# Optimization experiments

Measured on AMD Instinct MI355X. Metric: run time of the kernel, lower is better.

## Reference

```python
import jax, jax.numpy as jnp
import numpy as np

B, DIN, E, FACTOR, STEPS, NH = 2048, 1024, 1024, 16, 3, 8
DH = E // NH
EPS = 1e-5


def layernorm(x, g, b):
    m = x.mean(-1, keepdims=True)
    v = ((x - m) ** 2).mean(-1, keepdims=True)
    return (x - m) / jnp.sqrt(v + EPS) * g + b


def setup_inputs() -> dict:
    key = jax.random.key(0)
    ks = iter(jax.random.split(key, 32))
    r = lambda shape, s=0.02: jax.random.normal(next(ks), shape, dtype=jnp.float32) * s
    F = E * FACTOR
    return {
        "image_feat": jax.random.normal(next(ks), (B, DIN), dtype=jnp.float32),
        "text_feat": jax.random.normal(next(ks), (B, DIN), dtype=jnp.float32),
        # fusion block
        "fc1_w": r((F, DIN)), "fc1_b": jnp.zeros((F,), jnp.float32),
        "fc2_w": r((F, DIN)), "fc2_b": jnp.zeros((F,), jnp.float32),
        "fc3_w": r((E, F)), "fc3_b": jnp.zeros((E,), jnp.float32),
        "ln_g": jnp.ones((E,), jnp.float32), "ln_b": jnp.zeros((E,), jnp.float32),
        # per-step MHA + FFN + norms, stacked over STEPS
        "Wqkv": r((STEPS, 3 * E, E)), "bqkv": jnp.zeros((STEPS, 3 * E), jnp.float32),
        "Wo": r((STEPS, E, E)), "bo": jnp.zeros((STEPS, E), jnp.float32),
        "W1": r((STEPS, E, E)), "b1": jnp.zeros((STEPS, E), jnp.float32),
        "W2": r((STEPS, E, E)), "b2": jnp.zeros((STEPS, E), jnp.float32),
        "n1_g": jnp.ones((STEPS, E), jnp.float32), "n1_b": jnp.zeros((STEPS, E), jnp.float32),
        "n2_g": jnp.ones((STEPS, E), jnp.float32), "n2_b": jnp.zeros((STEPS, E), jnp.float32),
        # output projection
        "Wout": r((DIN, E)), "bout": jnp.zeros((DIN,), jnp.float32),
    }


def mha_step(q, ctx, Wqkv, bqkv, Wo, bo):
    # q: [B,E] (query len 1), ctx: [B,L,E]
    Wq, Wk, Wv = Wqkv[:E], Wqkv[E:2 * E], Wqkv[2 * E:]
    bq, bk, bv = bqkv[:E], bqkv[E:2 * E], bqkv[2 * E:]
    L = ctx.shape[1]
    qh = (q @ Wq.T + bq).reshape(B, NH, DH)
    kh = (ctx @ Wk.T + bk).reshape(B, L, NH, DH)
    vh = (ctx @ Wv.T + bv).reshape(B, L, NH, DH)
    scores = jnp.einsum("bhd,blhd->bhl", qh, kh) / jnp.sqrt(jnp.float32(DH))
    attn = jax.nn.softmax(scores, axis=-1)
    out = jnp.einsum("bhl,blhd->bhd", attn, vh).reshape(B, E)
    return out @ Wo.T + bo


def reference(image_feat, text_feat, fc1_w, fc1_b, fc2_w, fc2_b, fc3_w, fc3_b,
              ln_g, ln_b, Wqkv, bqkv, Wo, bo, W1, b1, W2, b2,
              n1_g, n1_b, n2_g, n2_b, Wout, bout):
    # fusion block (dropout = identity in eval)
    fused = (image_feat @ fc1_w.T + fc1_b) * (text_feat @ fc2_w.T + fc2_b)
    fused = layernorm(fused @ fc3_w.T + fc3_b, ln_g, ln_b)  # [B,E]
    ctx = fused[:, None, :]  # [B,1,E]
    x = fused
    for i in range(STEPS):
        attn = mha_step(x, ctx, Wqkv[i], bqkv[i], Wo[i], bo[i])
        x = x + layernorm(attn, n1_g[i], n1_b[i])
        ffn = jax.nn.relu(x @ W1[i].T + b1[i]) @ W2[i].T + b2[i]
        x = x + layernorm(ffn, n2_g[i], n2_b[i])
        ctx = jnp.concatenate([ctx, x[:, None, :]], axis=1)
    final_output = x @ Wout.T + bout  # [B,DIN]
    return final_output, ctx
```

## Files before the change

### kernel.cpp

```cpp
#include <hip/hip_runtime.h>

#define TB 256

typedef __attribute__((ext_vector_type(8))) short short8;
typedef __attribute__((ext_vector_type(4))) float f32x4;
typedef unsigned short u16;

constexpr int B_  = 2048;
constexpr int DIN = 1024;
constexpr int E   = 1024;
constexpr int F   = 16384;
constexpr int E3  = 3072;
constexpr int CH  = 4096;

struct Ptr8 { void* p[8]; };

__device__ __forceinline__ u16 f2bf(float f) {
  union { float f; unsigned u; } v; v.f = f;
  unsigned r = v.u + 0x7fffu + ((v.u >> 16) & 1u);
  return (u16)(r >> 16);
}
__device__ __forceinline__ float bf2f(u16 u) {
  union { unsigned u; float f; } v; v.u = ((unsigned)u) << 16;
  return v.f;
}

__device__ __forceinline__ void gload16(const void* g, void* l) {
  __builtin_amdgcn_global_load_lds(
      (const __attribute__((address_space(1))) void*)g,
      (__attribute__((address_space(3))) void*)l, 16, 0, 0);
}

__device__ __forceinline__ void tile_xy(int& tx, int& ty) {
  int gx = gridDim.x;
  int nwg = gx * gridDim.y;
  int wg = blockIdx.y * gx + blockIdx.x;
  if ((nwg & 7) == 0) wg = (wg & 7) * (nwg >> 3) + (wg >> 3);
  tx = wg % gx; ty = wg / gx;
}

__device__ __forceinline__ int swz16(int o) {
  return o ^ (((o >> 7) & 7) << 4);
}

__global__ __launch_bounds__(256) void cvt_kernel(const float* __restrict__ s,
                                                  u16* __restrict__ d, int n) {
  int i = (blockIdx.x * 256 + threadIdx.x) * 4;
  if (i >= n) return;
  float4 v = *(const float4*)&s[i];
  ushort4 o;
  o.x = f2bf(v.x); o.y = f2bf(v.y); o.z = f2bf(v.z); o.w = f2bf(v.w);
  *(ushort4*)&d[i] = o;
}

__global__ __launch_bounds__(256) void fill_kernel(float* p, int n, float v) {
  int i = blockIdx.x * 256 + threadIdx.x;
  if (i < n) p[i] = v;
}

__global__ __launch_bounds__(256) void relu_multi_kernel(
    Ptr8 ys, int ny, const float* __restrict__ bias, u16* __restrict__ out) {
  size_t i = ((size_t)blockIdx.x * 256 + threadIdx.x) * 4;
  int col = (int)(i & 1023);
  float4 b = *(const float4*)&bias[col];
  float a0 = b.x, a1 = b.y, a2 = b.z, a3 = b.w;
  for (int j = 0; j < ny; ++j) {
    float4 z = *(const float4*)&((const float*)ys.p[j])[i];
    a0 += z.x; a1 += z.y; a2 += z.z; a3 += z.w;
  }
  ushort4 o;
  o.x = f2bf(a0 > 0.f ? a0 : 0.f);
  o.y = f2bf(a1 > 0.f ? a1 : 0.f);
  o.z = f2bf(a2 > 0.f ? a2 : 0.f);
  o.w = f2bf(a3 > 0.f ? a3 : 0.f);
  *(ushort4*)&out[i] = o;
}

__global__ __launch_bounds__(256) void combine_out_kernel(
    Ptr8 ys, int ny, const float* __restrict__ bias, float* __restrict__ out) {
  size_t i = ((size_t)blockIdx.x * 256 + threadIdx.x) * 4;
  int col = (int)(i & 1023);
  float4 b = *(const float4*)&bias[col];
  float a0 = b.x, a1 = b.y, a2 = b.z, a3 = b.w;
  for (int j = 0; j < ny; ++j) {
    float4 z = *(const float4*)&((const float*)ys.p[j])[i];
    a0 += z.x; a1 += z.y; a2 += z.z; a3 += z.w;
  }
  out[i] = a0; out[i + 1] = a1; out[i + 2] = a2; out[i + 3] = a3;
}

template <int EPI>
__global__ __launch_bounds__(512, 2) void gemm256(
    const u16* __restrict__ A, int sA,
    const u16* __restrict__ Bw, int sB,
    const float* __restrict__ bias, const u16* __restrict__ gate,
    void* __restrict__ Out, Ptr8 pouts, int ldOut, int ksz) {
  __shared__ __align__(16) char smem[131072];
  const int tid = threadIdx.x, lane = tid & 63, w = tid >> 6;
  const int wm = w >> 2, wn = w & 3;
  int tx, ty; tile_xy(tx, ty);
  const int m0 = tx * 256, n0 = ty * 256;
  const int k0 = blockIdx.z * ksz;
  const int nt = ksz >> 5;
  const int lr = lane & 15;

  f32x4 acc[8][4] = {};

  auto stage = [&](const u16* __restrict__ G, int gs, int gr0, int kk, int tb, int j) {
    int P = j * 8192 + w * 1024 + lane * 16;
    int L = swz16(P);
    int pr = L >> 7, sub = (L >> 6) & 1, kb = L & 63;
    gload16(G + (size_t)(gr0 + pr * 2 + sub) * gs + kk + (kb >> 1),
            &smem[tb + P]);
  };
  auto rdA = [&](int tb, int mf) -> short8 {
    int r = wm * 128 + mf * 16 + lr;
    int o = (r >> 1) * 128 + (r & 1) * 64 + (lane >> 4) * 16;
    return *(const short8*)&smem[tb + swz16(o)];
  };
  auto rdB = [&](int tb, int nf) -> short8 {
    int r = wn * 64 + nf * 16 + lr;
    int o = (r >> 1) * 128 + (r & 1) * 64 + (lane >> 4) * 16;
    return *(const short8*)&smem[tb + swz16(o)];
  };
  auto slotA = [](int t) { return (t & 3) * 16384; };
  auto slotB = [](int t) { return 65536 + (t & 3) * 16384; };

#pragma unroll
  for (int j = 0; j < 2; ++j) stage(A, sA, m0, k0, slotA(0), j);
#pragma unroll
  for (int j = 0; j < 2; ++j) stage(Bw, sB, n0, k0, slotB(0), j);
  if (nt > 1) {
#pragma unroll
    for (int j = 0; j < 2; ++j) stage(A, sA, m0, k0 + 32, slotA(1), j);
#pragma unroll
    for (int j = 0; j < 2; ++j) stage(Bw, sB, n0, k0 + 32, slotB(1), j);
    asm volatile("s_waitcnt vmcnt(4)" ::: "memory");
  } else {
    asm volatile("s_waitcnt vmcnt(0)" ::: "memory");
  }
  __builtin_amdgcn_sched_barrier(0);
  __builtin_amdgcn_s_barrier();

  for (int t = 0; t < nt; ++t) {
    const int sa = slotA(t), sb = slotB(t);
    if (t + 2 < nt) {
#pragma unroll
      for (int j = 0; j < 2; ++j) stage(A, sA, m0, k0 + (t + 2) * 32, slotA(t + 2), j);
#pragma unroll
      for (int j = 0; j < 2; ++j) stage(Bw, sB, n0, k0 + (t + 2) * 32, slotB(t + 2), j);
    }
    short8 afr[8], bfr[4];
#pragma unroll
    for (int nf = 0; nf < 4; ++nf) bfr[nf] = rdB(sb, nf);
#pragma unroll
    for (int mf = 0; mf < 8; ++mf) afr[mf] = rdA(sa, mf);
    __builtin_amdgcn_s_setprio(1);
#pragma unroll
    for (int mf = 0; mf < 8; ++mf)
#pragma unroll
      for (int nf = 0; nf < 4; ++nf)
        acc[mf][nf] = __builtin_amdgcn_mfma_f32_16x16x32_bf16(
            afr[mf], bfr[nf], acc[mf][nf], 0, 0, 0);
    __builtin_amdgcn_s_setprio(0);
    if (t + 2 < nt) {
      asm volatile("s_waitcnt vmcnt(4)" ::: "memory");
    } else if (t + 1 < nt) {
      asm volatile("s_waitcnt vmcnt(0)" ::: "memory");
    }
    if (t + 1 < nt) {
      __builtin_amdgcn_sched_barrier(0);
      __builtin_amdgcn_s_barrier();
    }
  }

  if (EPI == 0) {
    float* Pf = (float*)pouts.p[blockIdx.z];
    const int rb = (lane >> 4) * 4;
#pragma unroll
    for (int mf = 0; mf < 8; ++mf) {
#pragma unroll
      for (int nf = 0; nf < 4; ++nf) {
        int row0 = m0 + wm * 128 + mf * 16 + rb;
        int col  = n0 + wn * 64 + nf * 16 + lr;
#pragma unroll
        for (int r = 0; r < 4; ++r)
          Pf[(size_t)(row0 + r) * ldOut + col] = acc[mf][nf][r];
      }
    }
  } else {
    __syncthreads();
    char* wbase = smem + w * 16384;
    const int rb = (lane >> 4) * 4;
    const int g4 = lane >> 4;
#pragma unroll
    for (int mf = 0; mf < 8; ++mf) {
      char* wmf = wbase + mf * 2048;
#pragma unroll
      for (int nf = 0; nf < 4; ++nf) {
        float bv = (bias == nullptr) ? 0.f : bias[n0 + wn * 64 + nf * 16 + lr];
        int pb = nf ^ g4;
#pragma unroll
        for (int r = 0; r < 4; ++r)
          *(u16*)&wmf[(rb + r) * 128 + pb * 32 + lr * 2] =
              f2bf(acc[mf][nf][r] + bv);
      }
      asm volatile("s_waitcnt lgkmcnt(0)" ::: "memory");
      __builtin_amdgcn_sched_barrier(0);
      int rrow = lane >> 2, wb = lane & 3;
      int pb2 = wb ^ (rrow >> 2);
      short8 v0 = *(const short8*)&wmf[rrow * 128 + pb2 * 32];
      short8 v1 = *(const short8*)&wmf[rrow * 128 + pb2 * 32 + 16];
      size_t gidx = (size_t)(m0 + wm * 128 + mf * 16 + rrow) * ldOut +
                    (n0 + wn * 64 + wb * 16);
      if (EPI == 4) {
        short8 g0 = *(const short8*)&gate[gidx];
        short8 g1 = *(const short8*)&gate[gidx + 8];
        short8 o0, o1;
#pragma unroll
        for (int j = 0; j < 8; ++j) {
          o0[j] = (short)f2bf(bf2f((u16)v0[j]) * bf2f((u16)g0[j]));
          o1[j] = (short)f2bf(bf2f((u16)v1[j]) * bf2f((u16)g1[j]));
        }
        *(short8*)((u16*)Out + gidx) = o0;
        *(short8*)((u16*)Out + gidx + 8) = o1;
      } else {
        *(short8*)((u16*)Out + gidx) = v0;
        *(short8*)((u16*)Out + gidx + 8) = v1;
      }
    }
  }
}

template <int EPI>
__global__ __launch_bounds__(TB) void gemm_bt(
    const u16* __restrict__ A, int sA,
    const u16* __restrict__ Bw, int sB,
    const float* __restrict__ bias, Ptr8 outs,
    int ldOut, int Kext, int ksz) {
  __shared__ u16 As[128 * 32];
  __shared__ u16 Bs[128 * 32];
  const int tid = threadIdx.x, lane = tid & 63, w = tid >> 6;
  const int wr = w >> 1, wc = w & 1;
  int tx, ty; tile_xy(tx, ty);
  const int m0 = tx * 128, n0 = ty * 128;
  const int k0 = blockIdx.z * ksz;
  const int kend = min(k0 + ksz, Kext);

  f32x4 acc[4][4] = {};
  const int lr = lane & 15, lk = (lane >> 4) * 8;

  for (int kk = k0; kk < kend; kk += 32) {
#pragma unroll
    for (int is = 0; is < 2; ++is) {
      int c = is * 256 + tid;
      int r = c >> 2, kc = (c & 3) << 3;
      size_t lb = (size_t)(is * 256 + w * 64) * 8;
      gload16(A  + (size_t)(m0 + r) * sA + kk + kc, &As[lb]);
      gload16(Bw + (size_t)(n0 + r) * sB + kk + kc, &Bs[lb]);
    }
    __syncthreads();
    short8 af[4], bfv[4];
#pragma unroll
    for (int m = 0; m < 4; ++m)
      af[m] = *(const short8*)&As[(wr * 64 + m * 16 + lr) * 32 + lk];
#pragma unroll
    for (int n = 0; n < 4; ++n)
      bfv[n] = *(const short8*)&Bs[(wc * 64 + n * 16 + lr) * 32 + lk];
#pragma unroll
    for (int m = 0; m < 4; ++m)
#pragma unroll
      for (int n = 0; n < 4; ++n)
        acc[m][n] = __builtin_amdgcn_mfma_f32_16x16x32_bf16(af[m], bfv[n], acc[m][n], 0, 0, 0);
    __syncthreads();
  }

  float* Of = (float*)outs.p[EPI == 0 ? blockIdx.z : 0];
  const int rbase = (lane >> 4) * 4;
#pragma unroll
  for (int m = 0; m < 4; ++m) {
#pragma unroll
    for (int n = 0; n < 4; ++n) {
      int row0 = m0 + wr * 64 + m * 16 + rbase;
      int col  = n0 + wc * 64 + n * 16 + lr;
      float bv = (bias == nullptr) ? 0.f : bias[col];
#pragma unroll
      for (int r = 0; r < 4; ++r) {
        float v = acc[m][n][r] + bv;
        size_t idx = (size_t)(row0 + r) * ldOut + col;
        if (EPI == 0) Of[idx] = v;
        else          ((u16*)Of)[idx] = f2bf(v);
      }
    }
  }
}

template <int EPI>
__global__ __launch_bounds__(TB) void gemm_wf32(
    const u16* __restrict__ A, int sA,
    const float* __restrict__ Bw, int sB,
    const float* __restrict__ bias, void* __restrict__ Out, int ldOut,
    int Kext, int ksz) {
  __shared__ u16 As[128 * 32];
  __shared__ u16 Bs[128 * 32];
  const int tid = threadIdx.x, lane = tid & 63, w = tid >> 6;
  const int wr = w >> 1, wc = w & 1;
  int tx, ty; tile_xy(tx, ty);
  const int m0 = tx * 128, n0 = ty * 128;
  const int k0 = blockIdx.z * ksz;
  const int kend = min(k0 + ksz, Kext);

  f32x4 acc[4][4] = {};
  const int lr = lane & 15, lk = (lane >> 4) * 8;

  for (int kk = k0; kk < kend; kk += 32) {
#pragma unroll
    for (int is = 0; is < 2; ++is) {
      int c = is * 256 + tid;
      int r = c >> 2, kc = (c & 3) << 3;
      gload16(A + (size_t)(m0 + r) * sA + kk + kc,
              &As[(size_t)(is * 256 + w * 64) * 8]);
    }
#pragma unroll
    for (int p = 0; p < 4; ++p) {
      int t = tid + p * 256;
      int r = t >> 3, c4 = (t & 7) << 2;
      float4 v = *(const float4*)&Bw[(size_t)(n0 + r) * sB + kk + c4];
      ushort4 o;
      o.x = f2bf(v.x); o.y = f2bf(v.y); o.z = f2bf(v.z); o.w = f2bf(v.w);
      *(ushort4*)&Bs[r * 32 + c4] = o;
    }
    __syncthreads();
    short8 af[4], bfv[4];
#pragma unroll
    for (int m = 0; m < 4; ++m)
      af[m] = *(const short8*)&As[(wr * 64 + m * 16 + lr) * 32 + lk];
#pragma unroll
    for (int n = 0; n < 4; ++n)
      bfv[n] = *(const short8*)&Bs[(wc * 64 + n * 16 + lr) * 32 + lk];
#pragma unroll
    for (int m = 0; m < 4; ++m)
#pragma unroll
      for (int n = 0; n < 4; ++n)
        acc[m][n] = __builtin_amdgcn_mfma_f32_16x16x32_bf16(af[m], bfv[n], acc[m][n], 0, 0, 0);
    __syncthreads();
  }

  const int rbase = (lane >> 4) * 4;
#pragma unroll
  for (int m = 0; m < 4; ++m) {
#pragma unroll
    for (int n = 0; n < 4; ++n) {
      int row0 = m0 + wr * 64 + m * 16 + rbase;
      int col  = n0 + wc * 64 + n * 16 + lr;
      float bv = (EPI == 3 || bias == nullptr) ? 0.f : bias[col];
#pragma unroll
      for (int r = 0; r < 4; ++r) {
        float v = acc[m][n][r] + bv;
        size_t idx = (size_t)(row0 + r) * ldOut + col;
        if (EPI == 0)      ((float*)Out)[idx] = v;
        else if (EPI == 1) ((u16*)Out)[idx] = f2bf(v);
        else if (EPI == 2) ((u16*)Out)[idx] = f2bf(v > 0.f ? v : 0.f);
        else               atomicAdd((float*)Out + idx, v);
      }
    }
  }
}

__global__ __launch_bounds__(TB) void gemm_dual_wf32(
    const u16* __restrict__ A1, const u16* __restrict__ A2, int sA,
    const float* __restrict__ B1, const float* __restrict__ B2, int sB,
    const float* __restrict__ bias1, const float* __restrict__ bias2,
    u16* __restrict__ Out, int ldOut, int K) {
  __shared__ u16 As1[128 * 32];
  __shared__ u16 As2[128 * 32];
  __shared__ u16 Bs1[128 * 32];
  __shared__ u16 Bs2[128 * 32];
  const int tid = threadIdx.x, lane = tid & 63, w = tid >> 6;
  const int wr = w >> 1, wc = w & 1;
  int tx, ty; tile_xy(tx, ty);
  const int m0 = tx * 128, n0 = ty * 128;

  f32x4 acc1[4][4] = {};
  f32x4 acc2[4][4] = {};
  const int lr = lane & 15, lk = (lane >> 4) * 8;

  for (int kk = 0; kk < K; kk += 32) {
#pragma unroll
    for (int is = 0; is < 2; ++is) {
      int c = is * 256 + tid;
      int r = c >> 2, kc = (c & 3) << 3;
      size_t lb = (size_t)(is * 256 + w * 64) * 8;
      gload16(A1 + (size_t)(m0 + r) * sA + kk + kc, &As1[lb]);
      gload16(A2 + (size_t)(m0 + r) * sA + kk + kc, &As2[lb]);
    }
#pragma unroll
    for (int p = 0; p < 4; ++p) {
      int t = tid + p * 256;
      int r = t >> 3, c4 = (t & 7) << 2;
      float4 v1 = *(const float4*)&B1[(size_t)(n0 + r) * sB + kk + c4];
      float4 v2 = *(const float4*)&B2[(size_t)(n0 + r) * sB + kk + c4];
      ushort4 o1, o2;
      o1.x = f2bf(v1.x); o1.y = f2bf(v1.y); o1.z = f2bf(v1.z); o1.w = f2bf(v1.w);
      o2.x = f2bf(v2.x); o2.y = f2bf(v2.y); o2.z = f2bf(v2.z); o2.w = f2bf(v2.w);
      *(ushort4*)&Bs1[r * 32 + c4] = o1;
      *(ushort4*)&Bs2[r * 32 + c4] = o2;
    }
    __syncthreads();
    short8 a1[4], a2[4], b1v[4], b2v[4];
#pragma unroll
    for (int m = 0; m < 4; ++m) {
      a1[m] = *(const short8*)&As1[(wr * 64 + m * 16 + lr) * 32 + lk];
      a2[m] = *(const short8*)&As2[(wr * 64 + m * 16 + lr) * 32 + lk];
    }
#pragma unroll
    for (int n = 0; n < 4; ++n) {
      b1v[n] = *(const short8*)&Bs1[(wc * 64 + n * 16 + lr) * 32 + lk];
      b2v[n] = *(const short8*)&Bs2[(wc * 64 + n * 16 + lr) * 32 + lk];
    }
#pragma unroll
    for (int m = 0; m < 4; ++m)
#pragma unroll
      for (int n = 0; n < 4; ++n) {
        acc1[m][n] = __builtin_amdgcn_mfma_f32_16x16x32_bf16(a1[m], b1v[n], acc1[m][n], 0, 0, 0);
        acc2[m][n] = __builtin_amdgcn_mfma_f32_16x16x32_bf16(a2[m], b2v[n], acc2[m][n], 0, 0, 0);
      }
    __syncthreads();
  }

  const int rbase = (lane >> 4) * 4;
#pragma unroll
  for (int m = 0; m < 4; ++m) {
#pragma unroll
    for (int n = 0; n < 4; ++n) {
      int row0 = m0 + wr * 64 + m * 16 + rbase;
      int col  = n0 + wc * 64 + n * 16 + lr;
      float bv1 = bias1[col], bv2 = bias2[col];
#pragma unroll
      for (int r = 0; r < 4; ++r) {
        float v = (acc1[m][n][r] + bv1) * (acc2[m][n][r] + bv2);
        Out[(size_t)(row0 + r) * ldOut + col] = f2bf(v);
      }
    }
  }
}

template <int MODE>
__global__ __launch_bounds__(256) void resln_kernel(
    Ptr8 ys, int ny, const float* __restrict__ preb,
    const float* __restrict__ g, const float* __restrict__ bp,
    float* __restrict__ x, u16* __restrict__ xb,
    float* __restrict__ ctxo, int ctxRow) {
  const int r = blockIdx.x, tid = threadIdx.x;
  const size_t base = (size_t)r * 1024 + tid * 4;
  float y[4] = {0.f, 0.f, 0.f, 0.f};
  for (int j = 0; j < ny; ++j) {
    float4 z = *(const float4*)&((const float*)ys.p[j])[base];
    y[0] += z.x; y[1] += z.y; y[2] += z.z; y[3] += z.w;
  }
  if (preb != nullptr) {
    float4 p4 = *(const float4*)&preb[tid * 4];
    y[0] += p4.x; y[1] += p4.y; y[2] += p4.z; y[3] += p4.w;
  }
  float s = y[0] + y[1] + y[2] + y[3];
  float q = y[0] * y[0] + y[1] * y[1] + y[2] * y[2] + y[3] * y[3];
  __shared__ float red[8];
  for (int o = 32; o; o >>= 1) { s += __shfl_xor(s, o); q += __shfl_xor(q, o); }
  int wv = tid >> 6;
  if ((tid & 63) == 0) { red[wv] = s; red[4 + wv] = q; }
  __syncthreads();
  s = red[0] + red[1] + red[2] + red[3];
  q = red[4] + red[5] + red[6] + red[7];
  float mean = s * (1.f / 1024.f);
  float var  = q * (1.f / 1024.f) - mean * mean;
  float rs   = rsqrtf(var + 1e-5f);
  float4 g4 = *(const float4*)&g[tid * 4];
  float4 b4 = *(const float4*)&bp[tid * 4];
  float gg[4] = {g4.x, g4.y, g4.z, g4.w};
  float bb[4] = {b4.x, b4.y, b4.z, b4.w};
  float xv[4];
#pragma unroll
  for (int j = 0; j < 4; ++j) {
    float val = (y[j] - mean) * rs * gg[j] + bb[j];
    xv[j] = (MODE == 0) ? val : x[base + j] + val;
  }
  *(float4*)&x[base] = make_float4(xv[0], xv[1], xv[2], xv[3]);
  ushort4 xo;
  xo.x = f2bf(xv[0]); xo.y = f2bf(xv[1]); xo.z = f2bf(xv[2]); xo.w = f2bf(xv[3]);
  *(ushort4*)&xb[base] = xo;
  if (MODE != 1) {
    size_t cb = ((size_t)r * 4 + ctxRow) * 1024 + tid * 4;
    *(float4*)&ctxo[cb] = make_float4(xv[0], xv[1], xv[2], xv[3]);
  }
}

__global__ __launch_bounds__(64) void attn_kernel(
    const u16* __restrict__ q, int qstride,
    const u16* __restrict__ kv, int kvstride, int voff,
    u16* __restrict__ out, int L) {
  const int b = blockIdx.x >> 3, h = blockIdx.x & 7;
  const int lane = threadIdx.x;
  const size_t qoff = (size_t)b * qstride + h * 128;
  float q0 = bf2f(q[qoff + lane]);
  float q1 = bf2f(q[qoff + 64 + lane]);
  float sc[3];
  for (int l = 0; l < L; ++l) {
    size_t kb = ((size_t)l * B_ + b) * kvstride + h * 128;
    float p = q0 * bf2f(kv[kb + lane]) + q1 * bf2f(kv[kb + 64 + lane]);
    for (int o = 32; o; o >>= 1) p += __shfl_xor(p, o);
    sc[l] = p * 0.08838834764831843f;
  }
  float m = sc[0];
  for (int l = 1; l < L; ++l) m = fmaxf(m, sc[l]);
  float wsum = 0.f, wgt[3];
  for (int l = 0; l < L; ++l) { wgt[l] = expf(sc[l] - m); wsum += wgt[l]; }
  float inv = 1.f / wsum;
  float o0 = 0.f, o1 = 0.f;
  for (int l = 0; l < L; ++l) {
    size_t vb = ((size_t)l * B_ + b) * kvstride + voff + h * 128;
    o0 += wgt[l] * bf2f(kv[vb + lane]);
    o1 += wgt[l] * bf2f(kv[vb + 64 + lane]);
  }
  out[(size_t)b * 1024 + h * 128 + lane]      = f2bf(o0 * inv);
  out[(size_t)b * 1024 + h * 128 + 64 + lane] = f2bf(o1 * inv);
}

extern "C" void kernel_launch(void* const* d_in, const int* in_sizes, int n_in,
                              void* d_out, int out_size, void* d_ws, size_t ws_size,
                              hipStream_t stream) {
  (void)in_sizes; (void)n_in;
  const float* image = (const float*)d_in[0];
  const float* text  = (const float*)d_in[1];
  const float* fc1_w = (const float*)d_in[2];
  const float* fc1_b = (const float*)d_in[3];
  const float* fc2_w = (const float*)d_in[4];
  const float* fc2_b = (const float*)d_in[5];
  const float* fc3_w = (const float*)d_in[6];
  const float* fc3_b = (const float*)d_in[7];
  const float* ln_g  = (const float*)d_in[8];
  const float* ln_b  = (const float*)d_in[9];
  const float* Wqkv  = (const float*)d_in[10];
  const float* bqkv  = (const float*)d_in[11];
  const float* Wo    = (const float*)d_in[12];
  const float* bo    = (const float*)d_in[13];
  const float* W1    = (const float*)d_in[14];
  const float* b1    = (const float*)d_in[15];
  const float* W2    = (const float*)d_in[16];
  const float* b2    = (const float*)d_in[17];
  const float* n1_g  = (const float*)d_in[18];
  const float* n1_b  = (const float*)d_in[19];
  const float* n2_g  = (const float*)d_in[20];
  const float* n2_b  = (const float*)d_in[21];
  const float* WoutW = (const float*)d_in[22];
  const float* boutW = (const float*)d_in[23];

  float* outF   = (float*)d_out;
  float* ctxOut = outF + (size_t)B_ * DIN;
  char* ws = (char*)d_ws;

  auto cvt = [&](const float* s, u16* d, size_t n) {
    cvt_kernel<<<dim3((unsigned)((n + 1023) / 1024)), 256, 0, stream>>>(s, d, (int)n);
  };

  const size_t NEED_A = 232783872;
  if (ws_size >= NEED_A) {
    size_t off = 0;
    auto carve = [&](size_t bytes) -> char* {
      char* p = ws + off; off += (bytes + 255) & ~(size_t)255; return p;
    };
    u16* imgB  = (u16*)carve((size_t)B_ * DIN * 2);
    u16* txtB  = (u16*)carve((size_t)B_ * DIN * 2);
    u16* fc1B  = (u16*)carve((size_t)F * DIN * 2);
    u16* fc2B  = (u16*)carve((size_t)F * DIN * 2);
    u16* fc3B  = (u16*)carve((size_t)E * F * 2);
    u16* WqkvB = (u16*)carve((size_t)3 * E3 * E * 2);
    u16* WoB   = (u16*)carve((size_t)3 * E * E * 2);
    u16* W1B   = (u16*)carve((size_t)3 * E * E * 2);
    u16* W2B   = (u16*)carve((size_t)3 * E * E * 2);
    u16* WoutB = (u16*)carve((size_t)DIN * E * 2);
    char* U    = carve((size_t)B_ * F * 2);
    float* xF  = (float*)carve((size_t)B_ * E * 4);
    float* hF  = (float*)carve((size_t)B_ * E * 4);
    u16* fusedB = (u16*)U;
    u16* kvB    = (u16*)(U);
    u16* qB     = (u16*)(U + 25165824);
    u16* ctxB   = (u16*)(U + 37748736);
    u16* attnB  = (u16*)(U + 37748736 + 16777216);
    u16* h1B    = (u16*)(U + 37748736 + 16777216 + 4194304);
    u16* xbB    = (u16*)(U + 37748736 + 16777216 + 8388608);
    float* PA = (float*)fc1B;
    float* PB = (float*)(fc1B + 4194304);
    float* PC = (float*)(fc1B + 8388608);
    float* PD = (float*)(fc1B + 12582912);
    float* PE = (float*)fc2B;
    float* PF = (float*)(fc2B + 4194304);

    cvt(image, imgB, (size_t)B_ * DIN);
    cvt(text,  txtB, (size_t)B_ * DIN);
    cvt(fc1_w, fc1B, (size_t)F * DIN);
    cvt(fc2_w, fc2B, (size_t)F * DIN);
    cvt(fc3_w, fc3B, (size_t)E * F);
    cvt(Wqkv,  WqkvB, (size_t)3 * E3 * E);
    cvt(Wo,    WoB,   (size_t)3 * E * E);
    cvt(W1,    W1B,   (size_t)3 * E * E);
    cvt(W2,    W2B,   (size_t)3 * E * E);
    cvt(WoutW, WoutB, (size_t)DIN * E);

    Ptr8 dumb{};
    gemm256<1><<<dim3(B_ / 256, F / 256), 512, 0, stream>>>(
        txtB, DIN, fc2B, DIN, fc2_b, nullptr, fusedB, dumb, F, DIN);
    gemm256<4><<<dim3(B_ / 256, F / 256), 512, 0, stream>>>(
        imgB, DIN, fc1B, DIN, fc1_b, fusedB, fusedB, dumb, F, DIN);
    Ptr8 p8f{{xF, hF, PA, PB, PC, PD, PE, PF}};
    gemm256<0><<<dim3(B_ / 256, E / 256, 8), 512, 0, stream>>>(
        fusedB, F, fc3B, F, nullptr, nullptr, nullptr, p8f, E, F / 8);
    resln_kernel<0><<<B_, 256, 0, stream>>>(
        p8f, 8, fc3_b, ln_g, ln_b, xF, ctxB, ctxOut, 0);

    Ptr8 p4{{hF, outF, PA, PB, nullptr, nullptr, nullptr, nullptr}};
    for (int i = 0; i < 3; ++i) {
      int L = i + 1;
      Ptr8 qkv1{{kvB, nullptr, nullptr, nullptr, nullptr, nullptr, nullptr, nullptr}};
      gemm_bt<1><<<dim3(L * B_ / 128, 2 * E / 128), TB, 0, stream>>>(
          ctxB, E, WqkvB + (size_t)i * E3 * E + (size_t)E * E, E,
          bqkv + (size_t)i * E3 + E, qkv1, 2 * E, E, E);
      Ptr8 qkv2{{qB, nullptr, nullptr, nullptr, nullptr, nullptr, nullptr, nullptr}};
      gemm_bt<1><<<dim3(B_ / 128, E / 128), TB, 0, stream>>>(
          ctxB + (size_t)i * B_ * E, E, WqkvB + (size_t)i * E3 * E, E,
          bqkv + (size_t)i * E3, qkv2, E, E, E);
      attn_kernel<<<B_ * 8, 64, 0, stream>>>(qB, E, kvB, 2 * E, E, attnB, L);
      gemm_bt<0><<<dim3(B_ / 128, E / 128, 4), TB, 0, stream>>>(
          attnB, E, WoB + (size_t)i * E * E, E, nullptr, p4, E, E, E / 4);
      resln_kernel<1><<<B_, 256, 0, stream>>>(
          p4, 4, bo + (size_t)i * E, n1_g + (size_t)i * E, n1_b + (size_t)i * E,
          xF, xbB, nullptr, 0);
      gemm_bt<0><<<dim3(B_ / 128, E / 128, 4), TB, 0, stream>>>(
          xbB, E, W1B + (size_t)i * E * E, E, nullptr, p4, E, E, E / 4);
      relu_multi_kernel<<<B_ * E / 1024, 256, 0, stream>>>(
          p4, 4, b1 + (size_t)i * E, h1B);
      gemm_bt<0><<<dim3(B_ / 128, E / 128, 4), TB, 0, stream>>>(
          h1B, E, W2B + (size_t)i * E * E, E, nullptr, p4, E, E, E / 4);
      resln_kernel<2><<<B_, 256, 0, stream>>>(
          p4, 4, b2 + (size_t)i * E, n2_g + (size_t)i * E, n2_b + (size_t)i * E,
          xF, ctxB + (size_t)(i + 1) * B_ * E, ctxOut, i + 1);
    }

    Ptr8 pfin{{hF, PA, PB, PC, nullptr, nullptr, nullptr, nullptr}};
    gemm_bt<0><<<dim3(B_ / 128, DIN / 128, 4), TB, 0, stream>>>(
        ctxB + (size_t)3 * B_ * E, E, WoutB, E, nullptr, pfin, DIN, E, E / 4);
    combine_out_kernel<<<B_ * DIN / 1024, 256, 0, stream>>>(pfin, 4, boutW, outF);
    return;
  }

  size_t off = 0;
  auto carve = [&](size_t bytes) -> char* {
    char* p = ws + off; off += (bytes + 255) & ~(size_t)255; return p;
  };
  u16* imgB   = (u16*)carve((size_t)B_ * DIN * 2);
  u16* txtB   = (u16*)carve((size_t)B_ * DIN * 2);
  u16* fusedC = (u16*)carve((size_t)B_ * CH * 2);
  u16* qkvB   = (u16*)carve((size_t)3 * B_ * E3 * 2);
  u16* ctxB   = (u16*)carve((size_t)4 * B_ * E * 2);
  u16* attnB  = (u16*)carve((size_t)B_ * E * 2);
  u16* h1B    = (u16*)carve((size_t)B_ * E * 2);
  u16* xbB    = (u16*)carve((size_t)B_ * E * 2);
  float* xF   = (float*)carve((size_t)B_ * E * 4);
  float* hF   = (float*)carve((size_t)B_ * E * 4);

  if (off > ws_size) {
    fill_kernel<<<(out_size + 255) / 256, 256, 0, stream>>>(outF, out_size, 12345.0f);
    return;
  }

  cvt(image, imgB, (size_t)B_ * DIN);
  cvt(text,  txtB, (size_t)B_ * DIN);
  hipMemsetAsync(hF, 0, (size_t)B_ * E * 4, stream);

  for (int c = 0; c < F / CH; ++c) {
    gemm_dual_wf32<<<dim3(B_ / 128, CH / 128), TB, 0, stream>>>(
        imgB, txtB, DIN,
        fc1_w + (size_t)c * CH * DIN, fc2_w + (size_t)c * CH * DIN, DIN,
        fc1_b + (size_t)c * CH, fc2_b + (size_t)c * CH, fusedC, CH, DIN);
    gemm_wf32<3><<<dim3(B_ / 128, E / 128, 2), TB, 0, stream>>>(
        fusedC, CH, fc3_w + (size_t)c * CH, F, nullptr, hF, E, CH, CH / 2);
  }
  {
    Ptr8 y1{{hF, nullptr, nullptr, nullptr, nullptr, nullptr, nullptr, nullptr}};
    resln_kernel<0><<<B_, 256, 0, stream>>>(y1, 1, fc3_b, ln_g, ln_b, xF, ctxB, ctxOut, 0);
  }

  for (int i = 0; i < 3; ++i) {
    int L = i + 1;
    gemm_wf32<1><<<dim3(L * B_ / 128, E3 / 128), TB, 0, stream>>>(
        ctxB, E, Wqkv + (size_t)i * E3 * E, E, bqkv + (size_t)i * E3, qkvB, E3, E, E);
    attn_kernel<<<B_ * 8, 64, 0, stream>>>(
        qkvB + (size_t)(L - 1) * B_ * E3, E3, qkvB + 1024, E3, 1024, attnB, L);
    gemm_wf32<0><<<dim3(B_ / 128, E / 128), TB, 0, stream>>>(
        attnB, E, Wo + (size_t)i * E * E, E, bo + (size_t)i * E, hF, E, E, E);
    Ptr8 y1{{hF, nullptr, nullptr, nullptr, nullptr, nullptr, nullptr, nullptr}};
    resln_kernel<1><<<B_, 256, 0, stream>>>(
        y1, 1, nullptr, n1_g + (size_t)i * E, n1_b + (size_t)i * E, xF, xbB, nullptr, 0);
    gemm_wf32<2><<<dim3(B_ / 128, E / 128), TB, 0, stream>>>(
        xbB, E, W1 + (size_t)i * E * E, E, b1 + (size_t)i * E, h1B, E, E, E);
    gemm_wf32<0><<<dim3(B_ / 128, E / 128), TB, 0, stream>>>(
        h1B, E, W2 + (size_t)i * E * E, E, b2 + (size_t)i * E, hF, E, E, E);
    resln_kernel<2><<<B_, 256, 0, stream>>>(
        y1, 1, nullptr, n2_g + (size_t)i * E, n2_b + (size_t)i * E, xF,
        ctxB + (size_t)(i + 1) * B_ * E, ctxOut, i + 1);
  }
  gemm_wf32<0><<<dim3(B_ / 128, DIN / 128), TB, 0, stream>>>(
      ctxB + (size_t)3 * B_ * E, E, WoutW, E, boutW, outF, DIN, E, E);
}
```

Measured before the change: 850.7 us.

## Halve gemm256 LDS to double-buffer for higher occupancy; stage bf16 stores in gemm_bt

```diff
diff --git a/kernel.cpp b/kernel.cpp
--- a/kernel.cpp
+++ b/kernel.cpp
@@ -90,12 +90,12 @@
 }
 
 template <int EPI>
-__global__ __launch_bounds__(512, 2) void gemm256(
+__global__ __launch_bounds__(512, 4) void gemm256(
     const u16* __restrict__ A, int sA,
     const u16* __restrict__ Bw, int sB,
     const float* __restrict__ bias, const u16* __restrict__ gate,
     void* __restrict__ Out, Ptr8 pouts, int ldOut, int ksz) {
-  __shared__ __align__(16) char smem[131072];
+  __shared__ __align__(16) char smem[65536];
   const int tid = threadIdx.x, lane = tid & 63, w = tid >> 6;
   const int wm = w >> 2, wn = w & 3;
   int tx, ty; tile_xy(tx, ty);
@@ -123,32 +123,26 @@
     int o = (r >> 1) * 128 + (r & 1) * 64 + (lane >> 4) * 16;
     return *(const short8*)&smem[tb + swz16(o)];
   };
-  auto slotA = [](int t) { return (t & 3) * 16384; };
-  auto slotB = [](int t) { return 65536 + (t & 3) * 16384; };
-
-#pragma unroll
-  for (int j = 0; j < 2; ++j) stage(A, sA, m0, k0, slotA(0), j);
-#pragma unroll
-  for (int j = 0; j < 2; ++j) stage(Bw, sB, n0, k0, slotB(0), j);
-  if (nt > 1) {
-#pragma unroll
-    for (int j = 0; j < 2; ++j) stage(A, sA, m0, k0 + 32, slotA(1), j);
-#pragma unroll
-    for (int j = 0; j < 2; ++j) stage(Bw, sB, n0, k0 + 32, slotB(1), j);
-    asm volatile("s_waitcnt vmcnt(4)" ::: "memory");
-  } else {
-    asm volatile("s_waitcnt vmcnt(0)" ::: "memory");
-  }
+
+#pragma unroll
+  for (int j = 0; j < 2; ++j) stage(A, sA, m0, k0, 0, j);
+#pragma unroll
+  for (int j = 0; j < 2; ++j) stage(Bw, sB, n0, k0, 32768, j);
+  asm volatile("s_waitcnt vmcnt(0)" ::: "memory");
   __builtin_amdgcn_sched_barrier(0);
   __builtin_amdgcn_s_barrier();
 
+  int cur = 0;
   for (int t = 0; t < nt; ++t) {
-    const int sa = slotA(t), sb = slotB(t);
-    if (t + 2 < nt) {
-#pragma unroll
-      for (int j = 0; j < 2; ++j) stage(A, sA, m0, k0 + (t + 2) * 32, slotA(t + 2), j);
-#pragma unroll
-      for (int j = 0; j < 2; ++j) stage(Bw, sB, n0, k0 + (t + 2) * 32, slotB(t + 2), j);
+    const int sa = cur * 16384;
+    const int sb = 32768 + cur * 16384;
+    if (t + 1 < nt) {
+      const int sa2 = (cur ^ 1) * 16384;
+      const int sb2 = 32768 + (cur ^ 1) * 16384;
+#pragma unroll
+      for (int j = 0; j < 2; ++j) stage(A, sA, m0, k0 + (t + 1) * 32, sa2, j);
+#pragma unroll
+      for (int j = 0; j < 2; ++j) stage(Bw, sB, n0, k0 + (t + 1) * 32, sb2, j);
     }
     short8 afr[8], bfr[4];
 #pragma unroll
@@ -163,15 +157,12 @@
         acc[mf][nf] = __builtin_amdgcn_mfma_f32_16x16x32_bf16(
             afr[mf], bfr[nf], acc[mf][nf], 0, 0, 0);
     __builtin_amdgcn_s_setprio(0);
-    if (t + 2 < nt) {
-      asm volatile("s_waitcnt vmcnt(4)" ::: "memory");
-    } else if (t + 1 < nt) {
+    if (t + 1 < nt) {
       asm volatile("s_waitcnt vmcnt(0)" ::: "memory");
-    }
-    if (t + 1 < nt) {
       __builtin_amdgcn_sched_barrier(0);
       __builtin_amdgcn_s_barrier();
     }
+    cur ^= 1;
   }
 
   if (EPI == 0) {
@@ -190,12 +181,12 @@
     }
   } else {
     __syncthreads();
-    char* wbase = smem + w * 16384;
+    char* wbase = smem + w * 8192;
     const int rb = (lane >> 4) * 4;
     const int g4 = lane >> 4;
 #pragma unroll
     for (int mf = 0; mf < 8; ++mf) {
-      char* wmf = wbase + mf * 2048;
+      char* wmf = wbase + (mf & 3) * 2048;
 #pragma unroll
       for (int nf = 0; nf < 4; ++nf) {
         float bv = (bias == nullptr) ? 0.f : bias[n0 + wn * 64 + nf * 16 + lr];
@@ -228,6 +219,7 @@
         *(short8*)((u16*)Out + gidx) = v0;
         *(short8*)((u16*)Out + gidx + 8) = v1;
       }
+      __builtin_amdgcn_sched_barrier(0);
     }
   }
 }
@@ -275,22 +267,55 @@
     __syncthreads();
   }
 
-  float* Of = (float*)outs.p[EPI == 0 ? blockIdx.z : 0];
-  const int rbase = (lane >> 4) * 4;
-#pragma unroll
-  for (int m = 0; m < 4; ++m) {
-#pragma unroll
-    for (int n = 0; n < 4; ++n) {
-      int row0 = m0 + wr * 64 + m * 16 + rbase;
-      int col  = n0 + wc * 64 + n * 16 + lr;
-      float bv = (bias == nullptr) ? 0.f : bias[col];
-#pragma unroll
-      for (int r = 0; r < 4; ++r) {
-        float v = acc[m][n][r] + bv;
-        size_t idx = (size_t)(row0 + r) * ldOut + col;
-        if (EPI == 0) Of[idx] = v;
-        else          ((u16*)Of)[idx] = f2bf(v);
-      }
+  if (EPI == 0) {
+    float* Of = (float*)outs.p[blockIdx.z];
+    const int rbase = (lane >> 4) * 4;
+#pragma unroll
+    for (int m = 0; m < 4; ++m) {
+#pragma unroll
+      for (int n = 0; n < 4; ++n) {
+        int row0 = m0 + wr * 64 + m * 16 + rbase;
+        int col  = n0 + wc * 64 + n * 16 + lr;
+        float bv = (bias == nullptr) ? 0.f : bias[col];
+#pragma unroll
+        for (int r = 0; r < 4; ++r)
+          Of[(size_t)(row0 + r) * ldOut + col] = acc[m][n][r] + bv;
+      }
+    }
+  } else {
+    u16* Of = (u16*)outs.p[0];
+    __syncthreads();
+    char* slice = (w < 2) ? (char*)As + w * 4096 : (char*)Bs + (w - 2) * 4096;
+    const int rb2 = (lane >> 4) * 4;
+#pragma unroll
+    for (int mh = 0; mh < 2; ++mh) {
+#pragma unroll
+      for (int mm = 0; mm < 2; ++mm) {
+        int m = mh * 2 + mm;
+#pragma unroll
+        for (int n = 0; n < 4; ++n) {
+          int col = n * 16 + lr;
+          float bv = (bias == nullptr) ? 0.f : bias[n0 + wc * 64 + col];
+#pragma unroll
+          for (int r = 0; r < 4; ++r) {
+            int rl = mm * 16 + rb2 + r;
+            int bo = (col * 2) ^ ((rl & 7) << 4);
+            *(u16*)&slice[rl * 128 + bo] = f2bf(acc[m][n][r] + bv);
+          }
+        }
+      }
+      asm volatile("s_waitcnt lgkmcnt(0)" ::: "memory");
+      __builtin_amdgcn_sched_barrier(0);
+#pragma unroll
+      for (int s = 0; s < 4; ++s) {
+        int c = s * 64 + lane;
+        int rl = c >> 3;
+        int bo = (((c & 7) ^ (rl & 7)) << 4);
+        short8 v = *(const short8*)&slice[rl * 128 + bo];
+        size_t grow = (size_t)(m0 + wr * 64 + mh * 32 + rl);
+        *(short8*)&Of[grow * ldOut + n0 + wc * 64 + (c & 7) * 8] = v;
+      }
+      __builtin_amdgcn_sched_barrier(0);
     }
   }
 }
```

New measurement: 2.729 ms. 3.21x slower.
